# Performance work log

Measured on AMD Instinct MI355X. Metric: run time of the kernel, lower is better.

The kernel has to match this reference:

```python
import jax, jax.numpy as jnp
import numpy as np

EPS = 1e-08


def setup_inputs() -> dict:
    key = jax.random.key(0)
    B, D = 8192, 512
    student_output = jax.random.normal(key, (B, D), dtype=jnp.float32)
    return {"student_output": student_output}


def reference(student_output) -> jnp.ndarray:
    # F.normalize(p=2, dim=-1, eps=EPS): x / max(||x||, eps)
    norm = jnp.linalg.norm(student_output, axis=-1, keepdims=True)
    x = student_output / jnp.maximum(norm, EPS)

    n = x.shape[0]
    # Pairwise inner products; mask the diagonal with -1 (self-match)
    dots = jnp.matmul(x, x.T)  # [B, B]
    idx = jnp.arange(n)
    dots = dots.at[idx, idx].set(-1.0)
    I = jnp.argmax(dots, axis=1)  # nearest neighbor index per row

    # torch.nn.PairwiseDistance(2, eps): ||x1 - x2 + eps||_2
    diff = x - x[I] + EPS
    distances = jnp.linalg.norm(diff, axis=-1)  # [B]
    loss = -jnp.mean(jnp.log(distances + EPS))
    return loss
```

## Files before the change

kernel.cpp:

```cpp
#include <hip/hip_runtime.h>
#include <hip/hip_bf16.h>
#include <math.h>

#define D_DIM 512
#define TM    128
#define TN    256

typedef int i32x4 __attribute__((ext_vector_type(4)));
typedef unsigned long long u64;


__device__ inline u64 shfl_xor_u64(u64 x, int m) {
    int lo = __shfl_xor((int)(unsigned)(x & 0xFFFFFFFFull), m, 64);
    int hi = __shfl_xor((int)(unsigned)(x >> 32), m, 64);
    return ((u64)(unsigned)hi << 32) | (u64)(unsigned)lo;
}

__device__ inline void async16(unsigned char* lds, const unsigned char* g) {
    __builtin_amdgcn_global_load_lds(
        (const __attribute__((address_space(1))) void*)g,
        (__attribute__((address_space(3))) void*)lds,
        16, 0, 0);
}


__global__ __launch_bounds__(256) void normalize_rows(
        const float* __restrict__ in, unsigned char* __restrict__ xb,
        float* __restrict__ inv_norm, u64* __restrict__ best,
        float* __restrict__ acc, int* __restrict__ cnt) {
    const int row  = blockIdx.x * 4 + (threadIdx.x >> 6);
    const int lane = threadIdx.x & 63;
    if (blockIdx.x == 0 && threadIdx.x == 0) { acc[0] = 0.f; cnt[0] = 0; }
    const float4* rp = (const float4*)(in + (size_t)row * D_DIM) + lane * 2;
    float4 a = rp[0], b = rp[1];
    float s = a.x*a.x + a.y*a.y + a.z*a.z + a.w*a.w
            + b.x*b.x + b.y*b.y + b.z*b.z + b.w*b.w;
    #pragma unroll
    for (int m = 1; m <= 32; m <<= 1) s += __shfl_xor(s, m, 64);
    float inv = 1.0f / fmaxf(sqrtf(s), 1e-8f);
    if (lane == 0) {
        inv_norm[row] = inv;
        best[row] = 0ull;
    }
    float sc = inv * 127.0f;
    int q0 = __float2int_rn(a.x*sc), q1 = __float2int_rn(a.y*sc);
    int q2 = __float2int_rn(a.z*sc), q3 = __float2int_rn(a.w*sc);
    int q4 = __float2int_rn(b.x*sc), q5 = __float2int_rn(b.y*sc);
    int q6 = __float2int_rn(b.z*sc), q7 = __float2int_rn(b.w*sc);
    int lo = (q0 & 255) | ((q1 & 255) << 8) | ((q2 & 255) << 16) | ((q3 & 255) << 24);
    int hi = (q4 & 255) | ((q5 & 255) << 8) | ((q6 & 255) << 16) | ((q7 & 255) << 24);
    ((int2*)(xb + (size_t)row * D_DIM))[lane] = make_int2(lo, hi);
}


__global__ __launch_bounds__(256, 2) void gemm_argmax(
        const unsigned char* __restrict__ X, u64* __restrict__ best) {
    __shared__ unsigned char As[2][64 * TM];
    __shared__ unsigned char Bs[2][64 * TN];
    __shared__ u64 rmerge[TM * 2];
    __shared__ u64 cmerge[TN * 2];

    int l = blockIdx.x;
    int q = (int)(sqrtf((float)l / 16.0f + 0.25f) - 0.5f);
    while (16 * (q + 1) * (q + 2) <= l) ++q;
    while (16 * q * (q + 1) > l) --q;
    int rrem = l - 16 * q * (q + 1);
    int cw   = 8 * (q + 1);
    int c    = rrem / cw;
    int bi   = rrem - c * cw;
    int bj   = 4 * q + c;
    if (bi > 2 * bj + 1) return;
    const int m0 = bi * TM;
    const int n0 = bj * TN;

    const int t    = threadIdx.x;
    const int lane = t & 63;
    const int w    = t >> 6;
    const int wm   = w >> 1, wn = w & 1;
    const int qr   = lane & 15;
    const int quad = lane >> 4;

    const int srcsl = ((t & 3) ^ ((t >> 3) & 3)) * 16;
    const unsigned char* gA = X + (size_t)(m0 + (t >> 2)) * D_DIM + srcsl;
    const unsigned char* gB = X + (size_t)(n0 + (t >> 2)) * D_DIM + srcsl;

    #define STAGE(buf, k0)                                            \
        do {                                                          \
            _Pragma("unroll")                                         \
            for (int j = 0; j < 2; j++)                               \
                async16(&As[buf][j * 4096 + t * 16],                  \
                        gA + (size_t)(j * 64) * D_DIM + (k0));        \
            _Pragma("unroll")                                         \
            for (int j = 0; j < 4; j++)                               \
                async16(&Bs[buf][j * 4096 + t * 16],                  \
                        gB + (size_t)(j * 64) * D_DIM + (k0));        \
        } while (0)

    i32x4 accm[4][8];
    #pragma unroll
    for (int mi = 0; mi < 4; mi++)
        #pragma unroll
        for (int ni = 0; ni < 8; ni++)
            accm[mi][ni] = (i32x4){0, 0, 0, 0};

    const int rdsl = (quad ^ ((qr >> 1) & 3)) * 16;

    STAGE(0, 0);
    #pragma unroll
    for (int t8 = 0; t8 < 8; t8++) {
        const int cur = t8 & 1;
        if (t8 < 7) {
            STAGE(cur ^ 1, (t8 + 1) * 64);
            asm volatile("s_waitcnt vmcnt(6)" ::: "memory");
        } else {
            asm volatile("s_waitcnt vmcnt(0)" ::: "memory");
        }
        __builtin_amdgcn_s_barrier();

        i32x4 av[4], bv[8];
        const unsigned char* pA = &As[cur][(wm * 64 + qr) * 64 + rdsl];
        const unsigned char* pB = &Bs[cur][(wn * 128 + qr) * 64 + rdsl];
        #pragma unroll
        for (int mi = 0; mi < 4; mi++)
            av[mi] = *(const i32x4*)(pA + mi * 1024);
        #pragma unroll
        for (int ni = 0; ni < 8; ni++)
            bv[ni] = *(const i32x4*)(pB + ni * 1024);
        #pragma unroll
        for (int mi = 0; mi < 4; mi++)
            #pragma unroll
            for (int ni = 0; ni < 8; ni++)
                accm[mi][ni] = __builtin_amdgcn_mfma_i32_16x16x64_i8(
                    av[mi], bv[ni], accm[mi][ni], 0, 0, 0);

        asm volatile("" ::: "memory");
        __builtin_amdgcn_s_barrier();
    }
    #undef STAGE

    const int colg_base = n0 + wn * 128 + qr;
    #pragma unroll
    for (int mi = 0; mi < 4; mi++) {
        #pragma unroll
        for (int r = 0; r < 4; r++) {
            const int rowl = wm * 64 + mi * 16 + quad * 4 + r;
            const int rowg = m0 + rowl;
            u64 key = 0ull;
            #pragma unroll
            for (int ni = 0; ni < 8; ni++) {
                int colg = colg_base + ni * 16;
                if (colg == rowg) continue;
                unsigned bd = (unsigned)accm[mi][ni][r] + 0x80000000u;
                u64 k = ((u64)bd << 32) | (u64)(0xFFFFFFFFu - (unsigned)colg);
                key = key > k ? key : k;
            }
            #pragma unroll
            for (int m = 1; m <= 8; m <<= 1) {
                u64 o = shfl_xor_u64(key, m);
                key = key > o ? key : o;
            }
            if (qr == 0) rmerge[rowl * 2 + wn] = key;
        }
    }

    #pragma unroll
    for (int ni = 0; ni < 8; ni++) {
        const int colg = colg_base + ni * 16;
        u64 key = 0ull;
        #pragma unroll
        for (int mi = 0; mi < 4; mi++) {
            #pragma unroll
            for (int r = 0; r < 4; r++) {
                int rowg = m0 + wm * 64 + mi * 16 + quad * 4 + r;
                if (rowg == colg) continue;
                unsigned bd = (unsigned)accm[mi][ni][r] + 0x80000000u;
                u64 k = ((u64)bd << 32) | (u64)(0xFFFFFFFFu - (unsigned)rowg);
                key = key > k ? key : k;
            }
        }
        u64 o = shfl_xor_u64(key, 16); key = key > o ? key : o;
        o     = shfl_xor_u64(key, 32); key = key > o ? key : o;
        if (quad == 0) cmerge[(wn * 128 + ni * 16 + qr) * 2 + wm] = key;
    }
    __syncthreads();
    if (t < TM) {
        u64 a = rmerge[t * 2], b = rmerge[t * 2 + 1];
        u64 k = a > b ? a : b;
        atomicMax(&best[m0 + t], k);
    }
    {
        u64 ca = cmerge[t * 2], cb = cmerge[t * 2 + 1];
        u64 ck = ca > cb ? ca : cb;
        atomicMax(&best[n0 + t], ck);
    }
}


__global__ __launch_bounds__(256) void neighbor_reduce(
        const float* __restrict__ in, const float* __restrict__ inv_norm,
        const u64* __restrict__ best, float* __restrict__ acc,
        int* __restrict__ cnt, float* __restrict__ out, int B) {
    const int wave = threadIdx.x >> 6;
    const int lane = threadIdx.x & 63;
    float lsum = 0.f;
    #pragma unroll
    for (int rr = 0; rr < 8; rr++) {
        const int row = blockIdx.x * 32 + wave * 8 + rr;
        u64 k   = best[row];
        int nbr = (int)(0xFFFFFFFFu - (unsigned)(k & 0xFFFFFFFFull));
        float ir  = inv_norm[row];
        float inb = inv_norm[nbr];
        const float4* rp = (const float4*)(in + (size_t)row * D_DIM) + lane * 2;
        const float4* np = (const float4*)(in + (size_t)nbr * D_DIM) + lane * 2;
        float4 r0 = rp[0], r1 = rp[1], q0 = np[0], q1 = np[1];
        float d0 = r0.x*ir - q0.x*inb + 1e-8f, d1 = r0.y*ir - q0.y*inb + 1e-8f;
        float d2 = r0.z*ir - q0.z*inb + 1e-8f, d3 = r0.w*ir - q0.w*inb + 1e-8f;
        float d4 = r1.x*ir - q1.x*inb + 1e-8f, d5 = r1.y*ir - q1.y*inb + 1e-8f;
        float d6 = r1.z*ir - q1.z*inb + 1e-8f, d7 = r1.w*ir - q1.w*inb + 1e-8f;
        float s = d0*d0 + d1*d1 + d2*d2 + d3*d3 + d4*d4 + d5*d5 + d6*d6 + d7*d7;
        #pragma unroll
        for (int m = 1; m <= 32; m <<= 1) s += __shfl_xor(s, m, 64);
        if (lane == 0) lsum += logf(sqrtf(s) + 1e-8f);
    }
    __shared__ float sb[4];
    if (lane == 0) sb[wave] = lsum;
    __syncthreads();
    if (threadIdx.x == 0) {
        float partial = sb[0] + sb[1] + sb[2] + sb[3];
        atomicAdd(acc, partial);
        __threadfence();
        int done = atomicAdd(cnt, 1);
        if (done == gridDim.x - 1) {
            __threadfence();
            float tot = atomicAdd(acc, 0.0f);
            out[0] = -tot / (float)B;
        }
    }
}


extern "C" void kernel_launch(void* const* d_in, const int* in_sizes, int n_in,
                              void* d_out, int out_size, void* d_ws, size_t ws_size,
                              hipStream_t stream) {
    const float* in = (const float*)d_in[0];
    const int B = in_sizes[0] / D_DIM;
    const int nblk = 16 * 8 * 9;

    char* w = (char*)d_ws;
    unsigned char* xb = (unsigned char*)w;
    float* invn = (float*)(w + (size_t)B * D_DIM);
    u64*   best = (u64*)(w + (size_t)B * D_DIM + (size_t)B * 4);
    float* acc  = (float*)(w + (size_t)B * D_DIM + (size_t)B * 4 + (size_t)B * 8);
    int*   cnt  = (int*)(acc + 1);
    float* out  = (float*)d_out;

    normalize_rows<<<B / 4, 256, 0, stream>>>(in, xb, invn, best, acc, cnt);
    gemm_argmax<<<nblk, 256, 0, stream>>>(xb, best);
    neighbor_reduce<<<B / 32, 256, 0, stream>>>(in, invn, best, acc, cnt, out, B);
}
```

Baseline: 121.0 us.

## Split GEMM tile across 8 waves and pack argmax keys into 32 bits

Launches the int8 GEMM-argmax kernel with 512 threads, so eight waves each own a 64x64 sub-tile instead of four waves each owning 64x128. This halves per-wave accumulator registers and allows up to 4 blocks per CU, aiming for more latency hiding. The staging now issues three async loads per thread per k-step. The argmax epilogue packs the biased 24-bit int dot product with an 8-bit local index into one 32-bit key. That halves shuffle traffic and shared-memory use, and the key is expanded back to the 64-bit form only for the global atomicMax. Correctness relies on |dot| staying below 2^23, which holds for 512 dimensions with int8 values up to 127.

After: 109.3 us. 1.11x faster.

```diff
diff --git a/kernel.cpp b/kernel.cpp
--- a/kernel.cpp
+++ b/kernel.cpp
@@ -9,12 +9,6 @@
 typedef int i32x4 __attribute__((ext_vector_type(4)));
 typedef unsigned long long u64;
 
-
-__device__ inline u64 shfl_xor_u64(u64 x, int m) {
-    int lo = __shfl_xor((int)(unsigned)(x & 0xFFFFFFFFull), m, 64);
-    int hi = __shfl_xor((int)(unsigned)(x >> 32), m, 64);
-    return ((u64)(unsigned)hi << 32) | (u64)(unsigned)lo;
-}
 
 __device__ inline void async16(unsigned char* lds, const unsigned char* g) {
     __builtin_amdgcn_global_load_lds(
@@ -53,12 +47,13 @@
 }
 
 
-__global__ __launch_bounds__(256, 2) void gemm_argmax(
+__global__ __launch_bounds__(512, 4) void gemm_argmax(
         const unsigned char* __restrict__ X, u64* __restrict__ best) {
-    __shared__ unsigned char As[2][64 * TM];
-    __shared__ unsigned char Bs[2][64 * TN];
-    __shared__ u64 rmerge[TM * 2];
-    __shared__ u64 cmerge[TN * 2];
+    __shared__ unsigned char smem[49152];
+    unsigned char* As0 = smem;
+    unsigned char* Bs0 = smem + 16384;
+    unsigned int* rmerge = (unsigned int*)smem;
+    unsigned int* cmerge = (unsigned int*)(smem + 2048);
 
     int l = blockIdx.x;
     int q = (int)(sqrtf((float)l / 16.0f + 0.25f) - 0.5f);
@@ -76,31 +71,28 @@
     const int t    = threadIdx.x;
     const int lane = t & 63;
     const int w    = t >> 6;
-    const int wm   = w >> 1, wn = w & 1;
+    const int wm   = w >> 2;
+    const int wn   = w & 3;
     const int qr   = lane & 15;
     const int quad = lane >> 4;
 
     const int srcsl = ((t & 3) ^ ((t >> 3) & 3)) * 16;
-    const unsigned char* gA = X + (size_t)(m0 + (t >> 2)) * D_DIM + srcsl;
-    const unsigned char* gB = X + (size_t)(n0 + (t >> 2)) * D_DIM + srcsl;
-
-    #define STAGE(buf, k0)                                            \
-        do {                                                          \
-            _Pragma("unroll")                                         \
-            for (int j = 0; j < 2; j++)                               \
-                async16(&As[buf][j * 4096 + t * 16],                  \
-                        gA + (size_t)(j * 64) * D_DIM + (k0));        \
-            _Pragma("unroll")                                         \
-            for (int j = 0; j < 4; j++)                               \
-                async16(&Bs[buf][j * 4096 + t * 16],                  \
-                        gB + (size_t)(j * 64) * D_DIM + (k0));        \
+    const unsigned char* gA  = X + (size_t)(m0 + (t >> 2)) * D_DIM + srcsl;
+    const unsigned char* gB  = X + (size_t)(n0 + (t >> 2)) * D_DIM + srcsl;
+    const unsigned char* gB2 = gB + (size_t)128 * D_DIM;
+
+    #define STAGE(buf, k0)                                        \
+        do {                                                      \
+            async16(As0 + (buf) * 8192 + t * 16, gA + (k0));      \
+            async16(Bs0 + (buf) * 16384 + t * 16, gB + (k0));     \
+            async16(Bs0 + (buf) * 16384 + 8192 + t * 16, gB2 + (k0)); \
         } while (0)
 
-    i32x4 accm[4][8];
+    i32x4 accm[4][4];
     #pragma unroll
     for (int mi = 0; mi < 4; mi++)
         #pragma unroll
-        for (int ni = 0; ni < 8; ni++)
+        for (int ni = 0; ni < 4; ni++)
             accm[mi][ni] = (i32x4){0, 0, 0, 0};
 
     const int rdsl = (quad ^ ((qr >> 1) & 3)) * 16;
@@ -111,25 +103,25 @@
         const int cur = t8 & 1;
         if (t8 < 7) {
             STAGE(cur ^ 1, (t8 + 1) * 64);
-            asm volatile("s_waitcnt vmcnt(6)" ::: "memory");
+            asm volatile("s_waitcnt vmcnt(3)" ::: "memory");
         } else {
             asm volatile("s_waitcnt vmcnt(0)" ::: "memory");
         }
         __builtin_amdgcn_s_barrier();
 
-        i32x4 av[4], bv[8];
-        const unsigned char* pA = &As[cur][(wm * 64 + qr) * 64 + rdsl];
-        const unsigned char* pB = &Bs[cur][(wn * 128 + qr) * 64 + rdsl];
+        i32x4 av[4], bv[4];
+        const unsigned char* pA = As0 + cur * 8192  + (wm * 64 + qr) * 64 + rdsl;
+        const unsigned char* pB = Bs0 + cur * 16384 + (wn * 64 + qr) * 64 + rdsl;
         #pragma unroll
         for (int mi = 0; mi < 4; mi++)
             av[mi] = *(const i32x4*)(pA + mi * 1024);
         #pragma unroll
-        for (int ni = 0; ni < 8; ni++)
+        for (int ni = 0; ni < 4; ni++)
             bv[ni] = *(const i32x4*)(pB + ni * 1024);
         #pragma unroll
         for (int mi = 0; mi < 4; mi++)
             #pragma unroll
-            for (int ni = 0; ni < 8; ni++)
+            for (int ni = 0; ni < 4; ni++)
                 accm[mi][ni] = __builtin_amdgcn_mfma_i32_16x16x64_i8(
                     av[mi], bv[ni], accm[mi][ni], 0, 0, 0);
 
@@ -138,60 +130,75 @@
     }
     #undef STAGE
 
-    const int colg_base = n0 + wn * 128 + qr;
+    const int colg_base = n0 + wn * 64 + qr;
+
     #pragma unroll
     for (int mi = 0; mi < 4; mi++) {
         #pragma unroll
         for (int r = 0; r < 4; r++) {
             const int rowl = wm * 64 + mi * 16 + quad * 4 + r;
             const int rowg = m0 + rowl;
-            u64 key = 0ull;
-            #pragma unroll
-            for (int ni = 0; ni < 8; ni++) {
-                int colg = colg_base + ni * 16;
-                if (colg == rowg) continue;
-                unsigned bd = (unsigned)accm[mi][ni][r] + 0x80000000u;
-                u64 k = ((u64)bd << 32) | (u64)(0xFFFFFFFFu - (unsigned)colg);
+            unsigned key = 0u;
+            #pragma unroll
+            for (int ni = 0; ni < 4; ni++) {
+                const int colg = colg_base + ni * 16;
+                const unsigned lcol = (unsigned)(wn * 64 + ni * 16 + qr);
+                unsigned k = (((unsigned)accm[mi][ni][r] + 0x800000u) << 8)
+                           | (255u - lcol);
+                k = (colg == rowg) ? 0u : k;
                 key = key > k ? key : k;
             }
             #pragma unroll
             for (int m = 1; m <= 8; m <<= 1) {
-                u64 o = shfl_xor_u64(key, m);
+                unsigned o = (unsigned)__shfl_xor((int)key, m, 64);
                 key = key > o ? key : o;
             }
-            if (qr == 0) rmerge[rowl * 2 + wn] = key;
-        }
-    }
-
-    #pragma unroll
-    for (int ni = 0; ni < 8; ni++) {
+            if (qr == 0) rmerge[rowl * 4 + wn] = key;
+        }
+    }
+
+    #pragma unroll
+    for (int ni = 0; ni < 4; ni++) {
         const int colg = colg_base + ni * 16;
-        u64 key = 0ull;
+        unsigned key = 0u;
         #pragma unroll
         for (int mi = 0; mi < 4; mi++) {
             #pragma unroll
             for (int r = 0; r < 4; r++) {
-                int rowg = m0 + wm * 64 + mi * 16 + quad * 4 + r;
-                if (rowg == colg) continue;
-                unsigned bd = (unsigned)accm[mi][ni][r] + 0x80000000u;
-                u64 k = ((u64)bd << 32) | (u64)(0xFFFFFFFFu - (unsigned)rowg);
+                const unsigned lrow = (unsigned)(wm * 64 + mi * 16 + quad * 4 + r);
+                const int rowg = m0 + (int)lrow;
+                unsigned k = (((unsigned)accm[mi][ni][r] + 0x800000u) << 8)
+                           | (255u - lrow);
+                k = (rowg == colg) ? 0u : k;
                 key = key > k ? key : k;
             }
         }
-        u64 o = shfl_xor_u64(key, 16); key = key > o ? key : o;
-        o     = shfl_xor_u64(key, 32); key = key > o ? key : o;
-        if (quad == 0) cmerge[(wn * 128 + ni * 16 + qr) * 2 + wm] = key;
+        unsigned o = (unsigned)__shfl_xor((int)key, 16, 64);
+        key = key > o ? key : o;
+        o = (unsigned)__shfl_xor((int)key, 32, 64);
+        key = key > o ? key : o;
+        if (quad == 0) cmerge[(wn * 64 + ni * 16 + qr) * 2 + wm] = key;
     }
     __syncthreads();
+
     if (t < TM) {
-        u64 a = rmerge[t * 2], b = rmerge[t * 2 + 1];
-        u64 k = a > b ? a : b;
-        atomicMax(&best[m0 + t], k);
-    }
-    {
-        u64 ca = cmerge[t * 2], cb = cmerge[t * 2 + 1];
-        u64 ck = ca > cb ? ca : cb;
-        atomicMax(&best[n0 + t], ck);
+        unsigned a0 = rmerge[t * 4], a1 = rmerge[t * 4 + 1];
+        unsigned a2 = rmerge[t * 4 + 2], a3 = rmerge[t * 4 + 3];
+        unsigned k01 = a0 > a1 ? a0 : a1;
+        unsigned k23 = a2 > a3 ? a2 : a3;
+        unsigned k = k01 > k23 ? k01 : k23;
+        unsigned bd32 = (k >> 8) + 0x7F800000u;
+        unsigned colg = (unsigned)(n0 + 255) - (k & 255u);
+        u64 kk = ((u64)bd32 << 32) | (u64)(0xFFFFFFFFu - colg);
+        atomicMax(&best[m0 + t], kk);
+    }
+    if (t < TN) {
+        unsigned c0 = cmerge[t * 2], c1 = cmerge[t * 2 + 1];
+        unsigned k = c0 > c1 ? c0 : c1;
+        unsigned bd32 = (k >> 8) + 0x7F800000u;
+        unsigned rowg = (unsigned)(m0 + 255) - (k & 255u);
+        u64 kk = ((u64)bd32 << 32) | (u64)(0xFFFFFFFFu - rowg);
+        atomicMax(&best[n0 + t], kk);
     }
 }
 
@@ -255,6 +262,6 @@
     float* out  = (float*)d_out;
 
     normalize_rows<<<B / 4, 256, 0, stream>>>(in, xb, invn, best, acc, cnt);
-    gemm_argmax<<<nblk, 256, 0, stream>>>(xb, best);
+    gemm_argmax<<<nblk, 512, 0, stream>>>(xb, best);
     neighbor_reduce<<<B / 32, 256, 0, stream>>>(in, invn, best, acc, cnt, out, B);
 }
```
